# Optimization experiments

Measured on AMD Instinct MI355X. Metric: run time of the kernel, lower is better.

Reference implementation:

```python
import jax, jax.numpy as jnp
import numpy as np

EPS = 1e-5  # torch LayerNorm default


def _lstm_layer(x, Wih, Whh, bih, bhh):
    """Batched multi-weight LSTM layer.
    x: (N, T, I); Wih: (N, 4H, I); Whh: (N, 4H, H); bih, bhh: (N, 4H).
    Gate order matches PyTorch: i, f, g, o.
    Returns (hs: (N, T, H), h_last: (N, H)).
    """
    N, T, _ = x.shape
    H = Whh.shape[-1]
    # Precompute input projections for all timesteps (high-intensity GEMM).
    xW = jnp.einsum('nti,ngi->ntg', x, Wih) + (bih + bhh)[:, None, :]  # (N, T, 4H)

    def step(carry, xt):
        h, c = carry
        gates = xt + jnp.einsum('nh,ngh->ng', h, Whh)  # (N, 4H)
        i, f, g, o = jnp.split(gates, 4, axis=-1)
        i = jax.nn.sigmoid(i)
        f = jax.nn.sigmoid(f)
        g = jnp.tanh(g)
        o = jax.nn.sigmoid(o)
        c = f * c + i * g
        h = o * jnp.tanh(c)
        return (h, c), h

    h0 = jnp.zeros((N, H), dtype=x.dtype)
    c0 = jnp.zeros((N, H), dtype=x.dtype)
    (h_last, _), hs = jax.lax.scan(step, (h0, c0), jnp.swapaxes(xW, 0, 1))
    return jnp.swapaxes(hs, 0, 1), h_last


def _layer_norm(x, gamma, beta):
    mu = jnp.mean(x, axis=-1, keepdims=True)
    var = jnp.mean(jnp.square(x - mu), axis=-1, keepdims=True)
    return (x - mu) * jax.lax.rsqrt(var + EPS) * gamma + beta


def setup_inputs() -> dict:
    key = jax.random.key(0)
    N, T, I, H = 128, 512, 32, 256
    ks = jax.random.split(key, 10)
    k = 1.0 / np.sqrt(H)  # torch LSTM init scale
    u = lambda kk, shape: jax.random.uniform(kk, shape, jnp.float32, -k, k)
    return {
        'x': jax.random.normal(ks[0], (N, T, I), jnp.float32),
        # layer 0 (input I -> H)
        'Wih0': u(ks[1], (N, 4 * H, I)),
        'Whh0': u(ks[2], (N, 4 * H, H)),
        'bih0': u(ks[3], (N, 4 * H)),
        'bhh0': u(ks[4], (N, 4 * H)),
        # layer 1 (H -> H)
        'Wih1': u(ks[5], (N, 4 * H, H)),
        'Whh1': u(ks[6], (N, 4 * H, H)),
        'bih1': u(ks[7], (N, 4 * H)),
        'bhh1': u(ks[8], (N, 4 * H)),
        # LayerNorm params
        'gamma': jnp.ones((H,), jnp.float32),
        'beta': jnp.zeros((H,), jnp.float32),
    }


def reference(x, Wih0, Whh0, bih0, bhh0, Wih1, Whh1, bih1, bhh1, gamma, beta):
    # Eval-mode forward: Dropout layers are identity.
    hs0, _ = _lstm_layer(x, Wih0, Whh0, bih0, bhh0)      # (N, T, H)
    _, h_last = _lstm_layer(hs0, Wih1, Whh1, bih1, bhh1)  # (N, H) = top-layer final hidden state
    return _layer_norm(h_last, gamma, beta)               # (N, H)
```

## Files before the change

kernel.cpp:

```cpp
#include <hip/hip_runtime.h>
#include <hip/hip_bf16.h>


typedef _Float16 half2_t __attribute__((ext_vector_type(2)));
typedef _Float16 half8_t __attribute__((ext_vector_type(8)));
typedef float floatx4 __attribute__((ext_vector_type(4)));

__device__ __forceinline__ unsigned pk(float a, float b) {
  half2_t h = { (_Float16)a, (_Float16)b };
  return __builtin_bit_cast(unsigned, h);
}
__device__ __forceinline__ float fdot2(unsigned w, unsigned h, float c) {
  return __builtin_amdgcn_fdot2(__builtin_bit_cast(half2_t, w),
                                __builtin_bit_cast(half2_t, h), c, false);
}
__device__ __forceinline__ float h2f(unsigned short u) {
  return (float)__builtin_bit_cast(_Float16, u);
}
__device__ __forceinline__ unsigned short f2h(float f) {
  return __builtin_bit_cast(unsigned short, (_Float16)f);
}
__device__ __forceinline__ float sigmf(float x) {
  return __builtin_amdgcn_rcpf(1.f + __expf(-x));
}
__device__ __forceinline__ float tanh_(float x) {
  return 2.f * sigmf(2.f * x) - 1.f;
}
__device__ __forceinline__ floatx4 mfma16(half8_t a, half8_t b, floatx4 c) {
  return __builtin_amdgcn_mfma_f32_16x16x32_f16(a, b, c, 0, 0, 0);
}
__device__ __forceinline__ unsigned rlane(unsigned v, int l) {
  return (unsigned)__builtin_amdgcn_readlane((int)v, l);
}

template<int K, int KT, bool AF16>
__global__ __launch_bounds__(256)
void gemm_xw(const void* __restrict__ Ap, const float* __restrict__ Bp,
             unsigned short* __restrict__ Cp)
{
  __shared__ unsigned short As[128][KT + 8];
  __shared__ unsigned short Bs[128][KT + 8];
  const int tid = threadIdx.x;
  const int node = blockIdx.y;
  const int mt = blockIdx.x >> 3;
  const int nt = blockIdx.x & 7;
  const int lane = tid & 63, wv = tid >> 6;
  const int wr = wv >> 1, wc = wv & 1;
  const int lm = lane & 15, lk = (lane >> 4) * 8;

  floatx4 zero = {0.f, 0.f, 0.f, 0.f};
  floatx4 acc[4][4];
#pragma unroll
  for (int i = 0; i < 4; ++i)
#pragma unroll
    for (int j = 0; j < 4; ++j) acc[i][j] = zero;

  for (int kt = 0; kt < K; kt += KT) {
    if (AF16) {
      const unsigned short* A = (const unsigned short*)Ap + (size_t)node * 512 * K;
      const int CPR = KT / 8;
#pragma unroll
      for (int c = tid; c < 128 * CPR; c += 256) {
        int r = c / CPR, cc = (c % CPR) * 8;
        *(uint4*)&As[r][cc] =
            *(const uint4*)(A + (size_t)(mt * 128 + r) * K + kt + cc);
      }
    } else {
      const float* A = (const float*)Ap + (size_t)node * 512 * K;
      const int CPR = KT / 4;
#pragma unroll
      for (int c = tid; c < 128 * CPR; c += 256) {
        int r = c / CPR, cc = (c % CPR) * 4;
        float4 v = *(const float4*)(A + (size_t)(mt * 128 + r) * K + kt + cc);
        uint2 p = make_uint2(pk(v.x, v.y), pk(v.z, v.w));
        *(uint2*)&As[r][cc] = p;
      }
    }
    {
      const float* B = Bp + (size_t)node * 1024 * K;
      const int CPR = KT / 4;
#pragma unroll
      for (int c = tid; c < 128 * CPR; c += 256) {
        int r = c / CPR, cc = (c % CPR) * 4;
        float4 v = *(const float4*)(B + (size_t)(nt * 128 + r) * K + kt + cc);
        uint2 p = make_uint2(pk(v.x, v.y), pk(v.z, v.w));
        *(uint2*)&Bs[r][cc] = p;
      }
    }
    __syncthreads();
#pragma unroll
    for (int ks = 0; ks < KT / 32; ++ks) {
      half8_t af[4], bf[4];
#pragma unroll
      for (int i = 0; i < 4; ++i)
        af[i] = *(const half8_t*)&As[wr * 64 + i * 16 + lm][ks * 32 + lk];
#pragma unroll
      for (int j = 0; j < 4; ++j)
        bf[j] = *(const half8_t*)&Bs[wc * 64 + j * 16 + lm][ks * 32 + lk];
#pragma unroll
      for (int i = 0; i < 4; ++i)
#pragma unroll
        for (int j = 0; j < 4; ++j)
          acc[i][j] = mfma16(af[i], bf[j], acc[i][j]);
    }
    __syncthreads();
  }
  unsigned short* C = Cp + (size_t)node * 512 * 1024;
#pragma unroll
  for (int i = 0; i < 4; ++i)
#pragma unroll
    for (int j = 0; j < 4; ++j)
#pragma unroll
      for (int r = 0; r < 4; ++r) {
        int row = mt * 128 + wr * 64 + i * 16 + (lane >> 4) * 4 + r;
        int col = nt * 128 + wc * 64 + j * 16 + lm;
        C[(size_t)row * 1024 + col] = f2h(acc[i][j][r]);
      }
}

#define VWP 96

template<bool WRITE_HS, bool FINAL>
__global__ __launch_bounds__(512, 2)
void lstm_rec(const unsigned short* __restrict__ xW,
              const float* __restrict__ Whh,
              const float* __restrict__ bih, const float* __restrict__ bhh,
              unsigned* __restrict__ hs,
              const float* __restrict__ gamma, const float* __restrict__ beta,
              float* __restrict__ out)
{
  __shared__ uint4 lw4[16][512];
  __shared__ __align__(16) unsigned short hbuf[2][256];
  __shared__ float fLN[256], sLN[256];
  __shared__ float redBuf[2];

  const int tid = threadIdx.x;
  const int lane = tid & 63;
  const int w = tid >> 6;
  const int n = blockIdx.x;
  const int lo = lane & 31;
  const bool lowHalf = lane < 32;
  const int d = w * 32 + lo;
  const int g0 = lowHalf ? d : 256 + d;
  const int g1 = lowHalf ? 512 + d : 768 + d;

  const float b0 = bih[n * 1024 + g0] + bhh[n * 1024 + g0];
  const float b1 = bih[n * 1024 + g1] + bhh[n * 1024 + g1];

  const float4* w0p = (const float4*)(Whh + ((size_t)n * 1024 + g0) * 256);
  const float4* w1p = (const float4*)(Whh + ((size_t)n * 1024 + g1) * 256);
  unsigned wv0[VWP], wv1[VWP];
#pragma unroll
  for (int i = 0; i < VWP / 2; ++i) {
    float4 v = w0p[i];
    wv0[2 * i] = pk(v.x, v.y);
    wv0[2 * i + 1] = pk(v.z, v.w);
    float4 u = w1p[i];
    wv1[2 * i] = pk(u.x, u.y);
    wv1[2 * i + 1] = pk(u.z, u.w);
  }
#pragma unroll
  for (int i = 0; i < 8; ++i) {
    float4 a = w0p[48 + 2 * i], b = w0p[49 + 2 * i];
    lw4[i][tid] = make_uint4(pk(a.x, a.y), pk(a.z, a.w), pk(b.x, b.y), pk(b.z, b.w));
    float4 c4 = w1p[48 + 2 * i], d4 = w1p[49 + 2 * i];
    lw4[8 + i][tid] = make_uint4(pk(c4.x, c4.y), pk(c4.z, c4.w), pk(d4.x, d4.y), pk(d4.z, d4.w));
  }

  if (tid < 32) ((uint4*)hbuf[0])[tid] = make_uint4(0, 0, 0, 0);
  float c = 0.f, hl = 0.f;
  const unsigned short* xwp = xW + (size_t)n * 512 * 1024;
  unsigned short xu0 = xwp[g0], xu1 = xwp[g1];
  __syncthreads();

  for (int t = 0; t < 512; ++t) {
    const uint2 hv = ((const uint2*)hbuf[t & 1])[lane];
    const unsigned short* xn = xwp + (size_t)((t + 1) & 511) * 1024;
    const unsigned short nxu0 = xn[g0], nxu1 = xn[g1];

    float aA0 = b0, aB0 = 0.f, aA1 = b1, aB1 = 0.f;
#pragma unroll
    for (int q = 0; q < 24; ++q) {
      const unsigned s0 = rlane(hv.x, 2 * q);
      const unsigned s1 = rlane(hv.y, 2 * q);
      const unsigned s2 = rlane(hv.x, 2 * q + 1);
      const unsigned s3 = rlane(hv.y, 2 * q + 1);
      aA0 = fdot2(wv0[4 * q + 0], s0, aA0); aA1 = fdot2(wv1[4 * q + 0], s0, aA1);
      aB0 = fdot2(wv0[4 * q + 1], s1, aB0); aB1 = fdot2(wv1[4 * q + 1], s1, aB1);
      aA0 = fdot2(wv0[4 * q + 2], s2, aA0); aA1 = fdot2(wv1[4 * q + 2], s2, aA1);
      aB0 = fdot2(wv0[4 * q + 3], s3, aB0); aB1 = fdot2(wv1[4 * q + 3], s3, aB1);
    }
#pragma unroll
    for (int q = 0; q < 8; ++q) {
      uint4 u0 = lw4[q][tid], u1 = lw4[8 + q][tid];
      const int l0 = 48 + 2 * q;
      const unsigned s0 = rlane(hv.x, l0);
      const unsigned s1 = rlane(hv.y, l0);
      const unsigned s2 = rlane(hv.x, l0 + 1);
      const unsigned s3 = rlane(hv.y, l0 + 1);
      aA0 = fdot2(u0.x, s0, aA0); aA1 = fdot2(u1.x, s0, aA1);
      aB0 = fdot2(u0.y, s1, aB0); aB1 = fdot2(u1.y, s1, aB1);
      aA0 = fdot2(u0.z, s2, aA0); aA1 = fdot2(u1.z, s2, aA1);
      aB0 = fdot2(u0.w, s3, aB0); aB1 = fdot2(u1.w, s3, aB1);
    }
    float a0 = (aA0 + aB0) + h2f(xu0);
    float a1 = (aA1 + aB1) + h2f(xu1);
    xu0 = nxu0; xu1 = nxu1;

    const float act0 = sigmf(a0);
    const float r1 = sigmf(lowHalf ? 2.f * a1 : a1);
    const float act1 = lowHalf ? 2.f * r1 - 1.f : r1;
    const float p0 = __shfl_xor(act0, 32, 64);
    const float p1 = __shfl_xor(act1, 32, 64);
    if (lowHalf) {
      c = p0 * c + act0 * act1;
      hl = p1 * tanh_(c);
      hbuf[(t + 1) & 1][d] = f2h(hl);
    }
    __syncthreads();
    if (WRITE_HS && tid < 128)
      hs[((size_t)n * 512 + t) * 128 + tid] = ((const unsigned*)hbuf[(t + 1) & 1])[tid];
  }

  if (FINAL) {
    if (lowHalf) fLN[d] = hl;
    __syncthreads();
    if (tid < 64) {
      float s = fLN[tid] + fLN[tid + 64] + fLN[tid + 128] + fLN[tid + 192];
      for (int off = 32; off > 0; off >>= 1) s += __shfl_down(s, off, 64);
      if (tid == 0) redBuf[0] = s * (1.f / 256.f);
    }
    __syncthreads();
    const float mu = redBuf[0];
    if (tid < 256) {
      const float dv = fLN[tid] - mu;
      sLN[tid] = dv * dv;
    }
    __syncthreads();
    if (tid < 64) {
      float s = sLN[tid] + sLN[tid + 64] + sLN[tid + 128] + sLN[tid + 192];
      for (int off = 32; off > 0; off >>= 1) s += __shfl_down(s, off, 64);
      if (tid == 0) redBuf[1] = s * (1.f / 256.f);
    }
    __syncthreads();
    if (tid < 256) {
      const float var = redBuf[1];
      out[(size_t)n * 256 + tid] =
          (fLN[tid] - mu) * rsqrtf(var + 1e-5f) * gamma[tid] + beta[tid];
    }
  }
}

extern "C" void kernel_launch(void* const* d_in, const int* in_sizes, int n_in,
                              void* d_out, int out_size, void* d_ws, size_t ws_size,
                              hipStream_t stream) {
  const float* x     = (const float*)d_in[0];
  const float* Wih0  = (const float*)d_in[1];
  const float* Whh0  = (const float*)d_in[2];
  const float* bih0  = (const float*)d_in[3];
  const float* bhh0  = (const float*)d_in[4];
  const float* Wih1  = (const float*)d_in[5];
  const float* Whh1  = (const float*)d_in[6];
  const float* bih1  = (const float*)d_in[7];
  const float* bhh1  = (const float*)d_in[8];
  const float* gamma = (const float*)d_in[9];
  const float* beta  = (const float*)d_in[10];
  float* out = (float*)d_out;

  unsigned short* xw  = (unsigned short*)d_ws;
  unsigned short* hs0 = (unsigned short*)((char*)d_ws + (size_t)134217728);

  gemm_xw<32, 32, false><<<dim3(32, 128), 256, 0, stream>>>(x, Wih0, xw);
  lstm_rec<true, false><<<128, 512, 0, stream>>>(xw, Whh0, bih0, bhh0,
                                                 (unsigned*)hs0, nullptr, nullptr,
                                                 nullptr);
  gemm_xw<256, 128, true><<<dim3(32, 128), 256, 0, stream>>>(hs0, Wih1, xw);
  lstm_rec<false, true><<<128, 512, 0, stream>>>(xw, Whh1, bih1, bhh1, nullptr,
                                                 gamma, beta, out);
}
```

Baseline: 2.442 ms.

## Use one thread per gate row in LSTM recurrence with 1024-thread blocks

The recurrent kernel now launches 1024 threads per sequence, with each thread owning a single gate row instead of two. Gate activations pass through shared memory and an extra barrier per timestep, replacing the cross-half shuffles. This halves the per-thread dot-product chain and adds more waves to hide latency. In exchange there are two barriers per step across 16 waves, and register pressure rises under launch_bounds(1024,4).

```diff
diff --git a/kernel.cpp b/kernel.cpp
--- a/kernel.cpp
+++ b/kernel.cpp
@@ -118,10 +118,10 @@
       }
 }
 
-#define VWP 96
+#define NV 96
 
 template<bool WRITE_HS, bool FINAL>
-__global__ __launch_bounds__(512, 2)
+__global__ __launch_bounds__(1024, 4)
 void lstm_rec(const unsigned short* __restrict__ xW,
               const float* __restrict__ Whh,
               const float* __restrict__ bih, const float* __restrict__ bhh,
@@ -129,92 +129,79 @@
               const float* __restrict__ gamma, const float* __restrict__ beta,
               float* __restrict__ out)
 {
-  __shared__ uint4 lw4[16][512];
+  __shared__ uint4 lw4[8][1024];
   __shared__ __align__(16) unsigned short hbuf[2][256];
-  __shared__ float fLN[256], sLN[256];
+  __shared__ float gBuf[768];
   __shared__ float redBuf[2];
 
   const int tid = threadIdx.x;
   const int lane = tid & 63;
-  const int w = tid >> 6;
   const int n = blockIdx.x;
-  const int lo = lane & 31;
-  const bool lowHalf = lane < 32;
-  const int d = w * 32 + lo;
-  const int g0 = lowHalf ? d : 256 + d;
-  const int g1 = lowHalf ? 512 + d : 768 + d;
-
-  const float b0 = bih[n * 1024 + g0] + bhh[n * 1024 + g0];
-  const float b1 = bih[n * 1024 + g1] + bhh[n * 1024 + g1];
-
-  const float4* w0p = (const float4*)(Whh + ((size_t)n * 1024 + g0) * 256);
-  const float4* w1p = (const float4*)(Whh + ((size_t)n * 1024 + g1) * 256);
-  unsigned wv0[VWP], wv1[VWP];
-#pragma unroll
-  for (int i = 0; i < VWP / 2; ++i) {
-    float4 v = w0p[i];
-    wv0[2 * i] = pk(v.x, v.y);
-    wv0[2 * i + 1] = pk(v.z, v.w);
-    float4 u = w1p[i];
-    wv1[2 * i] = pk(u.x, u.y);
-    wv1[2 * i + 1] = pk(u.z, u.w);
-  }
-#pragma unroll
-  for (int i = 0; i < 8; ++i) {
-    float4 a = w0p[48 + 2 * i], b = w0p[49 + 2 * i];
-    lw4[i][tid] = make_uint4(pk(a.x, a.y), pk(a.z, a.w), pk(b.x, b.y), pk(b.z, b.w));
-    float4 c4 = w1p[48 + 2 * i], d4 = w1p[49 + 2 * i];
-    lw4[8 + i][tid] = make_uint4(pk(c4.x, c4.y), pk(c4.z, c4.w), pk(d4.x, d4.y), pk(d4.z, d4.w));
+  const int g = tid;
+  const int grp = tid >> 8;
+  const int d = tid & 255;
+
+  const float bias = bih[n * 1024 + g] + bhh[n * 1024 + g];
+
+  const float4* wp = (const float4*)(Whh + ((size_t)n * 1024 + g) * 256);
+  unsigned wv[NV];
+#pragma unroll
+  for (int i = 0; i < NV / 2; ++i) {
+    float4 v = wp[i];
+    wv[2 * i] = pk(v.x, v.y);
+    wv[2 * i + 1] = pk(v.z, v.w);
+  }
+#pragma unroll
+  for (int j = 0; j < 8; ++j) {
+    float4 a = wp[48 + 2 * j], b = wp[49 + 2 * j];
+    lw4[j][tid] = make_uint4(pk(a.x, a.y), pk(a.z, a.w), pk(b.x, b.y), pk(b.z, b.w));
   }
 
   if (tid < 32) ((uint4*)hbuf[0])[tid] = make_uint4(0, 0, 0, 0);
   float c = 0.f, hl = 0.f;
   const unsigned short* xwp = xW + (size_t)n * 512 * 1024;
-  unsigned short xu0 = xwp[g0], xu1 = xwp[g1];
+  unsigned short xu = xwp[g];
   __syncthreads();
 
   for (int t = 0; t < 512; ++t) {
     const uint2 hv = ((const uint2*)hbuf[t & 1])[lane];
-    const unsigned short* xn = xwp + (size_t)((t + 1) & 511) * 1024;
-    const unsigned short nxu0 = xn[g0], nxu1 = xn[g1];
-
-    float aA0 = b0, aB0 = 0.f, aA1 = b1, aB1 = 0.f;
+    const unsigned short nxu = xwp[(size_t)((t + 1) & 511) * 1024 + g];
+
+    float a0 = bias, a1 = 0.f;
 #pragma unroll
     for (int q = 0; q < 24; ++q) {
       const unsigned s0 = rlane(hv.x, 2 * q);
       const unsigned s1 = rlane(hv.y, 2 * q);
       const unsigned s2 = rlane(hv.x, 2 * q + 1);
       const unsigned s3 = rlane(hv.y, 2 * q + 1);
-      aA0 = fdot2(wv0[4 * q + 0], s0, aA0); aA1 = fdot2(wv1[4 * q + 0], s0, aA1);
-      aB0 = fdot2(wv0[4 * q + 1], s1, aB0); aB1 = fdot2(wv1[4 * q + 1], s1, aB1);
-      aA0 = fdot2(wv0[4 * q + 2], s2, aA0); aA1 = fdot2(wv1[4 * q + 2], s2, aA1);
-      aB0 = fdot2(wv0[4 * q + 3], s3, aB0); aB1 = fdot2(wv1[4 * q + 3], s3, aB1);
-    }
-#pragma unroll
-    for (int q = 0; q < 8; ++q) {
-      uint4 u0 = lw4[q][tid], u1 = lw4[8 + q][tid];
-      const int l0 = 48 + 2 * q;
+      a0 = fdot2(wv[4 * q + 0], s0, a0);
+      a1 = fdot2(wv[4 * q + 1], s1, a1);
+      a0 = fdot2(wv[4 * q + 2], s2, a0);
+      a1 = fdot2(wv[4 * q + 3], s3, a1);
+    }
+#pragma unroll
+    for (int j = 0; j < 8; ++j) {
+      const uint4 u = lw4[j][tid];
+      const int l0 = 48 + 2 * j;
       const unsigned s0 = rlane(hv.x, l0);
       const unsigned s1 = rlane(hv.y, l0);
       const unsigned s2 = rlane(hv.x, l0 + 1);
       const unsigned s3 = rlane(hv.y, l0 + 1);
-      aA0 = fdot2(u0.x, s0, aA0); aA1 = fdot2(u1.x, s0, aA1);
-      aB0 = fdot2(u0.y, s1, aB0); aB1 = fdot2(u1.y, s1, aB1);
-      aA0 = fdot2(u0.z, s2, aA0); aA1 = fdot2(u1.z, s2, aA1);
-      aB0 = fdot2(u0.w, s3, aB0); aB1 = fdot2(u1.w, s3, aB1);
-    }
-    float a0 = (aA0 + aB0) + h2f(xu0);
-    float a1 = (aA1 + aB1) + h2f(xu1);
-    xu0 = nxu0; xu1 = nxu1;
-
-    const float act0 = sigmf(a0);
-    const float r1 = sigmf(lowHalf ? 2.f * a1 : a1);
-    const float act1 = lowHalf ? 2.f * r1 - 1.f : r1;
-    const float p0 = __shfl_xor(act0, 32, 64);
-    const float p1 = __shfl_xor(act1, 32, 64);
-    if (lowHalf) {
-      c = p0 * c + act0 * act1;
-      hl = p1 * tanh_(c);
+      a0 = fdot2(u.x, s0, a0);
+      a1 = fdot2(u.y, s1, a1);
+      a0 = fdot2(u.z, s2, a0);
+      a1 = fdot2(u.w, s3, a1);
+    }
+    const float a = (a0 + a1) + h2f(xu);
+    xu = nxu;
+
+    const float act = (grp == 2) ? tanh_(a) : sigmf(a);
+    if (grp) gBuf[tid - 256] = act;
+    __syncthreads();
+    if (grp == 0) {
+      const float f = gBuf[d], gg = gBuf[256 + d], o = gBuf[512 + d];
+      c = f * c + act * gg;
+      hl = o * tanh_(c);
       hbuf[(t + 1) & 1][d] = f2h(hl);
     }
     __syncthreads();
@@ -223,22 +210,22 @@
   }
 
   if (FINAL) {
-    if (lowHalf) fLN[d] = hl;
+    if (grp == 0) gBuf[d] = hl;
     __syncthreads();
     if (tid < 64) {
-      float s = fLN[tid] + fLN[tid + 64] + fLN[tid + 128] + fLN[tid + 192];
+      float s = gBuf[tid] + gBuf[tid + 64] + gBuf[tid + 128] + gBuf[tid + 192];
       for (int off = 32; off > 0; off >>= 1) s += __shfl_down(s, off, 64);
       if (tid == 0) redBuf[0] = s * (1.f / 256.f);
     }
     __syncthreads();
     const float mu = redBuf[0];
     if (tid < 256) {
-      const float dv = fLN[tid] - mu;
-      sLN[tid] = dv * dv;
+      const float dv = gBuf[tid] - mu;
+      gBuf[256 + tid] = dv * dv;
     }
     __syncthreads();
     if (tid < 64) {
-      float s = sLN[tid] + sLN[tid + 64] + sLN[tid + 128] + sLN[tid + 192];
+      float s = gBuf[256 + tid] + gBuf[320 + tid] + gBuf[384 + tid] + gBuf[448 + tid];
       for (int off = 32; off > 0; off >>= 1) s += __shfl_down(s, off, 64);
       if (tid == 0) redBuf[1] = s * (1.f / 256.f);
     }
@@ -246,7 +233,7 @@
     if (tid < 256) {
       const float var = redBuf[1];
       out[(size_t)n * 256 + tid] =
-          (fLN[tid] - mu) * rsqrtf(var + 1e-5f) * gamma[tid] + beta[tid];
+          (gBuf[tid] - mu) * rsqrtf(var + 1e-5f) * gamma[tid] + beta[tid];
     }
   }
 }
@@ -271,10 +258,10 @@
   unsigned short* hs0 = (unsigned short*)((char*)d_ws + (size_t)134217728);
 
   gemm_xw<32, 32, false><<<dim3(32, 128), 256, 0, stream>>>(x, Wih0, xw);
-  lstm_rec<true, false><<<128, 512, 0, stream>>>(xw, Whh0, bih0, bhh0,
-                                                 (unsigned*)hs0, nullptr, nullptr,
-                                                 nullptr);
+  lstm_rec<true, false><<<128, 1024, 0, stream>>>(xw, Whh0, bih0, bhh0,
+                                                  (unsigned*)hs0, nullptr, nullptr,
+                                                  nullptr);
   gemm_xw<256, 128, true><<<dim3(32, 128), 256, 0, stream>>>(hs0, Wih1, xw);
-  lstm_rec<false, true><<<128, 512, 0, stream>>>(xw, Whh1, bih1, bhh1, nullptr,
-                                                 gamma, beta, out);
-}
+  lstm_rec<false, true><<<128, 1024, 0, stream>>>(xw, Whh1, bih1, bhh1, nullptr,
+                                                  gamma, beta, out);
+}
```

Result: slower. 2.919 ms (+19.6%).
